# Performance work log

Hardware: AMD Instinct MI355X
Metric: run time of the kernel (lower is better)

The kernel has to match this reference:

```python
import jax, jax.numpy as jnp
import numpy as np

B, C, F, J = 64, 16, 2048, 25
EMBED, CLASSES, NJ = 64, 5, 12
AFFECT = slice(0, 12)
UNAFFECT = slice(12, 24)


def setup_inputs() -> dict:
    key = jax.random.key(0)
    k0, k1, k2, k3 = jax.random.split(key, 4)
    features = jax.random.normal(k0, (B, C, F, J), dtype=jnp.float32)
    W1 = jax.random.normal(k1, (EMBED, C, NJ), dtype=jnp.float32) * 0.05
    b1 = jnp.zeros((EMBED,), jnp.float32)
    W2 = jax.random.normal(k2, (EMBED, C, NJ), dtype=jnp.float32) * 0.05
    b2 = jnp.zeros((EMBED,), jnp.float32)
    Wl = jax.random.normal(k3, (CLASSES, 16 * EMBED), dtype=jnp.float32) * 0.02
    bl = jnp.zeros((CLASSES,), jnp.float32)
    return {"features": features, "W1": W1, "b1": b1, "W2": W2, "b2": b2, "Wl": Wl, "bl": bl}


def _stat_features(x, proto):
    # x: [b, c, f, j]; single sort shared by min/max/quantiles/median
    f = x.shape[-2]
    xs = jnp.sort(x, axis=-2)

    def quant(p):
        # torch.quantile linear interpolation
        pos = p * (f - 1)
        lo = int(np.floor(pos)); hi = int(np.ceil(pos)); frac = np.float32(pos - lo)
        return xs[..., lo, :] * (1.0 - frac) + xs[..., hi, :] * frac

    s1 = xs[..., 0, :]                       # min
    s2 = xs[..., -1, :]                      # max
    s3 = quant(0.25)
    s4 = xs[..., (f - 1) // 2, :]            # torch.median: lower middle element
    s5 = quant(0.75)
    s6 = jnp.mean(x, axis=-2)
    s7 = jnp.std(x, axis=-2, ddof=1)         # torch.std unbiased
    s8 = s2 - s1
    z = (x - s6[..., None, :]) / s7[..., None, :]
    if proto:
        s9 = jnp.mean(z ** 3, axis=-2)       # skew
    else:
        s9 = jnp.mean(z ** 4, axis=-2) - 3.0  # excess kurtosis
    return jnp.stack([s2, s3, s4, s5, s6, s7, s8, s9], axis=-2)  # [b, c, 8, j]


def _fuse(stat, W, b):
    # Conv2d kernel (1, joints) == contraction over (c, j) per stat row
    out = jnp.einsum('bcsj,ecj->bes', stat, W) + b[None, :, None]
    return out.reshape(out.shape[0], -1)  # flatten (embed, stats) like torch.flatten


def reference(features, W1, b1, W2, b2, Wl, bl):
    affected = features[:, :, :, AFFECT]
    unaffected = features[:, :, :, UNAFFECT]
    stat_af = _stat_features(affected, proto=False)
    stat_ua = _stat_features(unaffected, proto=False)
    # attn=False path (STAT_VA block disabled)
    stat1 = _stat_features(unaffected + affected, proto=True)
    _ = _fuse(stat1, W1, b1)  # stat1 branch only feeds CL loss (get_cl_loss=False)
    stat2 = jnp.concatenate([stat_af, stat_ua], axis=-2)  # [b, c, 16, j]
    flat2 = _fuse(stat2, W2, b2)                          # [b, 16*embed]
    logits = flat2 @ Wl.T + bl
    return logits
```

## Files before the change

kernel.cpp:

```cpp
#include <hip/hip_runtime.h>
#include <hip/hip_bf16.h>


#define F_LEN 2048
#define JTOT 25
#define STATS_PER_BC 192

__global__ __launch_bounds__(256) void stat_kernel(
    const float* __restrict__ Fp, float* __restrict__ stat2) {
  const int g = blockIdx.x;
  const int xcd = g & 7;
  const int mm = g >> 3;
  const int bc = xcd * 128 + mm / 6;
  const int grp = mm % 6;
  const int w = threadIdx.x >> 6;
  const int lane = threadIdx.x & 63;
  const int j = grp * 4 + w;

  const float* base =
      Fp + ((size_t)bc * F_LEN + (size_t)lane * 32) * JTOT + j;

  float x[32];
#pragma unroll
  for (int e = 0; e < 32; ++e) x[e] = base[e * JTOT];

  float sum = 0.f;
#pragma unroll
  for (int e = 0; e < 32; ++e) sum += x[e];
#pragma unroll
  for (int off = 32; off; off >>= 1) sum += __shfl_xor(sum, off, 64);
  const float m = sum * (1.0f / 2048.0f);

  float c2 = 0.f, c4 = 0.f;
#pragma unroll
  for (int e = 0; e < 32; ++e) {
    float d = x[e] - m;
    float dd = d * d;
    c2 += dd;
    c4 += dd * dd;
  }
#pragma unroll
  for (int off = 32; off; off >>= 1) {
    c2 += __shfl_xor(c2, off, 64);
    c4 += __shfl_xor(c4, off, 64);
  }
  const float var = c2 * (1.0f / 2047.0f);
  const float sd = sqrtf(var);
  const float kurt = (c4 * (1.0f / 2048.0f)) / (var * var) - 3.0f;

#pragma unroll
  for (int kp = 1; kp <= 4; ++kp) {
    const int k = 1 << kp;
#pragma unroll
    for (int jp = kp - 1; jp >= 0; --jp) {
      const int st = 1 << jp;
#pragma unroll
      for (int e = 0; e < 32; ++e) {
        if ((e & st) == 0) {
          const bool up = ((e & k) == 0);
          float a = x[e], b = x[e + st];
          float lo = fminf(a, b), hi = fmaxf(a, b);
          x[e] = up ? lo : hi;
          x[e + st] = up ? hi : lo;
        }
      }
    }
  }

  unsigned curflip = 0u;
#pragma unroll
  for (int kp = 5; kp <= 10; ++kp) {
    const unsigned want = ((lane >> (kp - 5)) & 1) ? 0x80000000u : 0u;
    const unsigned fl = want ^ curflip;
    curflip = want;
#pragma unroll
    for (int e = 0; e < 32; ++e)
      x[e] = __uint_as_float(__float_as_uint(x[e]) ^ fl);
#pragma unroll
    for (int jp = kp - 1; jp >= 0; --jp) {
      const int st = 1 << jp;
      if (st >= 32) {
        const int mask = st >> 5;
        const bool keepmin = ((lane & mask) == 0);
#pragma unroll
        for (int e = 0; e < 32; ++e) {
          float o = __shfl_xor(x[e], mask, 64);
          x[e] = keepmin ? fminf(x[e], o) : fmaxf(x[e], o);
        }
      } else {
#pragma unroll
        for (int e = 0; e < 32; ++e) {
          if ((e & st) == 0) {
            float a = x[e], b = x[e + st];
            x[e] = fminf(a, b);
            x[e + st] = fmaxf(a, b);
          }
        }
      }
    }
  }
#pragma unroll
  for (int e = 0; e < 32; ++e)
    x[e] = __uint_as_float(__float_as_uint(x[e]) ^ curflip);

#pragma unroll
  for (int jp = 10; jp >= 0; --jp) {
    const int st = 1 << jp;
    if (st >= 32) {
      const int mask = st >> 5;
      const bool keepmin = ((lane & mask) == 0);
#pragma unroll
      for (int e = 0; e < 32; ++e) {
        float o = __shfl_xor(x[e], mask, 64);
        x[e] = keepmin ? fminf(x[e], o) : fmaxf(x[e], o);
      }
    } else {
#pragma unroll
      for (int e = 0; e < 32; ++e) {
        if ((e & st) == 0) {
          float a = x[e], b = x[e + st];
          x[e] = fminf(a, b);
          x[e + st] = fmaxf(a, b);
        }
      }
    }
  }

  const float mn    = __shfl(x[0], 0, 64);
  const float a511  = __shfl(x[31], 15, 64);
  const float a512  = __shfl(x[0], 16, 64);
  const float amed  = __shfl(x[31], 31, 64);
  const float a1535 = __shfl(x[31], 47, 64);
  const float a1536 = __shfl(x[0], 48, 64);
  const float mx    = __shfl(x[31], 63, 64);

  if (lane == 0) {
    const float q25 = 0.25f * a511 + 0.75f * a512;
    const float q75 = 0.75f * a1535 + 0.25f * a1536;
    const int jj = (j < 12) ? j : j - 12;
    const int sb = (j < 12) ? 0 : 8;
    float st[8] = {mx, q25, amed, q75, m, sd, mx - mn, kurt};
    float* o = stat2 + (bc * 16 + sb) * 12 + jj;
#pragma unroll
    for (int s = 0; s < 8; ++s) o[s * 12] = st[s];
  }
}

__global__ __launch_bounds__(256) void fuse_kernel(
    const float* __restrict__ stat2, const float* __restrict__ W2,
    const float* __restrict__ b2, const float* __restrict__ Wl,
    const float* __restrict__ bl, float* __restrict__ out) {
  __shared__ float s_stat[16 * STATS_PER_BC];
  __shared__ float s_flat[1024];
  __shared__ float s_red[4];

  const int b = blockIdx.x;
  const int t = threadIdx.x;

  for (int idx = t; idx < 16 * STATS_PER_BC; idx += 256)
    s_stat[idx] = stat2[b * (16 * STATS_PER_BC) + idx];
  __syncthreads();

  const int e = t & 63;
  const int q = t >> 6;
  float acc[4] = {0.f, 0.f, 0.f, 0.f};
  for (int c = 0; c < 16; ++c) {
    const float* wrow = W2 + (e * 16 + c) * 12;
    const float* srow = s_stat + c * STATS_PER_BC;
#pragma unroll
    for (int jj = 0; jj < 12; ++jj) {
      const float wv = wrow[jj];
#pragma unroll
      for (int ss = 0; ss < 4; ++ss)
        acc[ss] += srow[(q * 4 + ss) * 12 + jj] * wv;
    }
  }
  const float bb = b2[e];
#pragma unroll
  for (int ss = 0; ss < 4; ++ss)
    s_flat[e * 16 + q * 4 + ss] = acc[ss] + bb;
  __syncthreads();

  for (int k = 0; k < 5; ++k) {
    float p = 0.f;
    for (int i = t; i < 1024; i += 256) p += s_flat[i] * Wl[k * 1024 + i];
#pragma unroll
    for (int off = 32; off; off >>= 1) p += __shfl_down(p, off, 64);
    if ((t & 63) == 0) s_red[t >> 6] = p;
    __syncthreads();
    if (t == 0)
      out[b * 5 + k] = s_red[0] + s_red[1] + s_red[2] + s_red[3] + bl[k];
    __syncthreads();
  }
}

extern "C" void kernel_launch(void* const* d_in, const int* in_sizes, int n_in,
                              void* d_out, int out_size, void* d_ws,
                              size_t ws_size, hipStream_t stream) {
  const float* Fp = (const float*)d_in[0];
  const float* W2 = (const float*)d_in[3];
  const float* b2 = (const float*)d_in[4];
  const float* Wl = (const float*)d_in[5];
  const float* bl = (const float*)d_in[6];
  float* out = (float*)d_out;

  float* stat2 = (float*)d_ws;

  stat_kernel<<<6144, 256, 0, stream>>>(Fp, stat2);
  fuse_kernel<<<64, 256, 0, stream>>>(stat2, W2, b2, Wl, bl, out);
}
```

Measured before the change: 467.4 us.

## Replace final bitonic merge with LDS dump and merge-path order-statistic search

The full bitonic sort of each 2048-element column is stopped after forming a sorted half-ascending/half-descending bitonic sequence, which removes the final 11-stage merge. The cross-lane merge stages are rewritten with sign-flip tricks so each shuffle step is a single fminf against the negated partner. The two sorted halves are written to a swizzled LDS buffer, and a few lanes run an 11-step merge-path binary search to pull out the needed order statistics: quartile neighbours, median, min and max. This adds 32 KB of LDS per block, which may reduce occupancy, and adds serial dependent LDS reads in exchange for fewer shuffle and compare stages.

```diff
diff --git a/kernel.cpp b/kernel.cpp
--- a/kernel.cpp
+++ b/kernel.cpp
@@ -1,13 +1,19 @@
 #include <hip/hip_runtime.h>
 #include <hip/hip_bf16.h>
+#include <math.h>
 
 
 #define F_LEN 2048
 #define JTOT 25
 #define STATS_PER_BC 192
 
+__device__ __forceinline__ int swz(int i) {
+  return (i & ~31) | ((i + ((i >> 5) << 2)) & 31);
+}
+
 __global__ __launch_bounds__(256) void stat_kernel(
     const float* __restrict__ Fp, float* __restrict__ stat2) {
+  __shared__ float lds[4 * 2048];
   const int g = blockIdx.x;
   const int xcd = g & 7;
   const int mm = g >> 3;
@@ -16,6 +22,7 @@
   const int w = threadIdx.x >> 6;
   const int lane = threadIdx.x & 63;
   const int j = grp * 4 + w;
+  float* wlds = lds + w * 2048;
 
   const float* base =
       Fp + ((size_t)bc * F_LEN + (size_t)lane * 32) * JTOT + j;
@@ -59,62 +66,44 @@
         if ((e & st) == 0) {
           const bool up = ((e & k) == 0);
           float a = x[e], b = x[e + st];
-          float lo = fminf(a, b), hi = fmaxf(a, b);
-          x[e] = up ? lo : hi;
-          x[e + st] = up ? hi : lo;
+          float lo2 = fminf(a, b), hi2 = fmaxf(a, b);
+          x[e] = up ? lo2 : hi2;
+          x[e + st] = up ? hi2 : lo2;
         }
       }
     }
   }
 
-  unsigned curflip = 0u;
+  unsigned Fst = 0u;
 #pragma unroll
   for (int kp = 5; kp <= 10; ++kp) {
-    const unsigned want = ((lane >> (kp - 5)) & 1) ? 0x80000000u : 0u;
-    const unsigned fl = want ^ curflip;
-    curflip = want;
-#pragma unroll
-    for (int e = 0; e < 32; ++e)
-      x[e] = __uint_as_float(__float_as_uint(x[e]) ^ fl);
-#pragma unroll
-    for (int jp = kp - 1; jp >= 0; --jp) {
+    const unsigned d = ((lane >> (kp - 5)) & 1) ? 0x80000000u : 0u;
+#pragma unroll
+    for (int jp = kp - 1; jp >= 5; --jp) {
+      const int lm = 1 << (jp - 5);
+      const unsigned r = ((lane >> (jp - 5)) & 1) ? 0x80000000u : 0u;
+      const unsigned tgt = d ^ r;
+      const unsigned fl = tgt ^ Fst;
+      Fst = tgt;
+#pragma unroll
+      for (int e = 0; e < 32; ++e)
+        x[e] = __uint_as_float(__float_as_uint(x[e]) ^ fl);
+#pragma unroll
+      for (int e = 0; e < 32; ++e) {
+        float o = __shfl_xor(x[e], lm, 64);
+        x[e] = fminf(x[e], -o);
+      }
+    }
+    {
+      const unsigned fl = d ^ Fst;
+      Fst = d;
+#pragma unroll
+      for (int e = 0; e < 32; ++e)
+        x[e] = __uint_as_float(__float_as_uint(x[e]) ^ fl);
+    }
+#pragma unroll
+    for (int jp = (kp - 1 < 4 ? kp - 1 : 4); jp >= 0; --jp) {
       const int st = 1 << jp;
-      if (st >= 32) {
-        const int mask = st >> 5;
-        const bool keepmin = ((lane & mask) == 0);
-#pragma unroll
-        for (int e = 0; e < 32; ++e) {
-          float o = __shfl_xor(x[e], mask, 64);
-          x[e] = keepmin ? fminf(x[e], o) : fmaxf(x[e], o);
-        }
-      } else {
-#pragma unroll
-        for (int e = 0; e < 32; ++e) {
-          if ((e & st) == 0) {
-            float a = x[e], b = x[e + st];
-            x[e] = fminf(a, b);
-            x[e + st] = fmaxf(a, b);
-          }
-        }
-      }
-    }
-  }
-#pragma unroll
-  for (int e = 0; e < 32; ++e)
-    x[e] = __uint_as_float(__float_as_uint(x[e]) ^ curflip);
-
-#pragma unroll
-  for (int jp = 10; jp >= 0; --jp) {
-    const int st = 1 << jp;
-    if (st >= 32) {
-      const int mask = st >> 5;
-      const bool keepmin = ((lane & mask) == 0);
-#pragma unroll
-      for (int e = 0; e < 32; ++e) {
-        float o = __shfl_xor(x[e], mask, 64);
-        x[e] = keepmin ? fminf(x[e], o) : fmaxf(x[e], o);
-      }
-    } else {
 #pragma unroll
       for (int e = 0; e < 32; ++e) {
         if ((e & st) == 0) {
@@ -125,24 +114,69 @@
       }
     }
   }
-
-  const float mn    = __shfl(x[0], 0, 64);
-  const float a511  = __shfl(x[31], 15, 64);
-  const float a512  = __shfl(x[0], 16, 64);
-  const float amed  = __shfl(x[31], 31, 64);
-  const float a1535 = __shfl(x[31], 47, 64);
-  const float a1536 = __shfl(x[0], 48, 64);
-  const float mx    = __shfl(x[31], 63, 64);
+#pragma unroll
+  for (int e = 0; e < 32; ++e)
+    x[e] = __uint_as_float(__float_as_uint(x[e]) ^ Fst);
+
+  {
+    float4* dst4 = (float4*)wlds;
+#pragma unroll
+    for (int q = 0; q < 8; ++q) {
+      int wq = 8 * lane + ((q + lane) & 7);
+      dst4[wq] = make_float4(x[4 * q], x[4 * q + 1], x[4 * q + 2], x[4 * q + 3]);
+    }
+  }
+
+  const int kk = (lane == 0) ? 511
+               : (lane == 1) ? 512
+               : (lane == 2) ? 1023
+               : (lane == 3) ? 1535 : 1536;
+  const int mtot = kk + 1;
+  int lo = mtot - 1024; if (lo < 0) lo = 0;
+  int hi = (mtot < 1024) ? mtot : 1024;
+  for (int it = 0; it < 11; ++it) {
+    const bool act = lo < hi;
+    const int s = (lo + hi) >> 1;
+    const int sa = (s < 1023) ? s : 1023;
+    float Av = wlds[swz(sa)];
+    Av = (s < 1024) ? Av : INFINITY;
+    int bidx = mtot - s - 1;
+    bidx = bidx < 0 ? 0 : (bidx > 1023 ? 1023 : bidx);
+    const float Bv = wlds[swz(2047 - bidx)];
+    const bool gg = act && (Bv > Av);
+    if (gg) lo = s + 1;
+    else if (act) hi = s;
+  }
+  float val;
+  {
+    const int s = lo;
+    const int ia = (s - 1 < 0) ? 0 : s - 1;
+    const float fa = wlds[swz(ia)];
+    const float fromA = (s > 0) ? fa : -INFINITY;
+    const int bi = mtot - s - 1;
+    const int ib = (bi < 0) ? 0 : bi;
+    const float fb = wlds[swz(2047 - ib)];
+    const float fromB = (bi >= 0) ? fb : -INFINITY;
+    val = fmaxf(fromA, fromB);
+  }
+
+  const float a511  = __shfl(val, 0, 64);
+  const float a512  = __shfl(val, 1, 64);
+  const float amed  = __shfl(val, 2, 64);
+  const float a1535 = __shfl(val, 3, 64);
+  const float a1536 = __shfl(val, 4, 64);
 
   if (lane == 0) {
+    const float mn = fminf(wlds[swz(0)], wlds[swz(2047)]);
+    const float mx = fmaxf(wlds[swz(1023)], wlds[swz(1024)]);
     const float q25 = 0.25f * a511 + 0.75f * a512;
     const float q75 = 0.75f * a1535 + 0.25f * a1536;
     const int jj = (j < 12) ? j : j - 12;
     const int sb = (j < 12) ? 0 : 8;
-    float st[8] = {mx, q25, amed, q75, m, sd, mx - mn, kurt};
+    float st8[8] = {mx, q25, amed, q75, m, sd, mx - mn, kurt};
     float* o = stat2 + (bc * 16 + sb) * 12 + jj;
 #pragma unroll
-    for (int s = 0; s < 8; ++s) o[s * 12] = st[s];
+    for (int s2 = 0; s2 < 8; ++s2) o[s2 * 12] = st8[s2];
   }
 }
 
```

After: 454.9 us. 1.03x faster.
